# Kernel tuning notes

Hardware: AMD Instinct MI355X
Metric: run time of the kernel (lower is better)

Reference implementation:

```python
import jax, jax.numpy as jnp
import numpy as np

B, N, H = 32, 1024, 256
ALPHA = 0.2  # leaky relu slope
NEG_INF = -1e12


def setup_inputs() -> dict:
    key = jax.random.key(0)
    k1, k2, k3, k4, k5, k6 = jax.random.split(key, 6)
    inp = jax.random.normal(k1, (B, N, H), dtype=jnp.float32)
    A = (jax.random.uniform(k2, (B, N, N)) < 0.05).astype(jnp.float32)
    l = jnp.sort(jax.random.randint(k3, (B, 2), 0, N), axis=1)
    # xavier-uniform(gain=1.414) approximated; exact init values are irrelevant for correctness
    lim_w = 1.414 * np.sqrt(6.0 / (H + H))
    W_i = jax.random.uniform(k4, (H, H), minval=-lim_w, maxval=lim_w, dtype=jnp.float32)
    W_c = jax.random.uniform(k5, (H, H), minval=-lim_w, maxval=lim_w, dtype=jnp.float32)
    lim_a = 1.414 * np.sqrt(6.0 / (2 * H + 1))
    a = jax.random.uniform(k6, (2 * H, 1), minval=-lim_a, maxval=lim_a, dtype=jnp.float32)
    return {"inp": inp, "A": A, "l": l, "W_i": W_i, "W_c": W_c, "a": a}


def reference(inp, A, l, W_i, W_c, a):
    # eval mode: dropout is identity (training=False)
    n = inp.shape[1]
    h = inp.shape[2]
    Wh_i = jnp.einsum('bnh,he->bne', inp, W_i)
    Wh_c = jnp.einsum('bnh,he->bne', inp, W_c)
    # vectorized replacement of the per-batch Wh[index][i:j] = Wh_i[index][i:j] loop
    idx = jnp.arange(n)
    sel = (idx[None, :] >= l[:, 0:1]) & (idx[None, :] < l[:, 1:2])  # [B,N]
    Wh = jnp.where(sel[:, :, None], Wh_i, Wh_c)
    # additive attention scores
    Wh1 = Wh @ a[:h, :]  # [B,N,1]
    Wh2 = Wh @ a[h:, :]  # [B,N,1]
    A_ = A + jnp.eye(n, dtype=A.dtype)
    e = jax.nn.leaky_relu((Wh1 + jnp.swapaxes(Wh2, 1, 2)) * A_, ALPHA)
    att = jnp.where(A_ > 0, e, NEG_INF)
    att = jax.nn.softmax(att, axis=2)
    h_prime = jnp.einsum('bnm,bme->bne', att, Wh)
    return jax.nn.elu(h_prime)  # concat=True
```

## Files before the change

### kernel.cpp

```cpp
#include <hip/hip_runtime.h>
#include <hip/hip_bf16.h>
#include <stdint.h>

#define B_ 32
#define N_ 1024
#define H_ 256
#define PF_PITCH 520

typedef short bf16x8 __attribute__((ext_vector_type(8)));
typedef float floatx4 __attribute__((ext_vector_type(4)));

__device__ inline unsigned short f2bs(float x) {
    __hip_bfloat16 h = __float2bfloat16(x);
    return __builtin_bit_cast(unsigned short, h);
}

__global__ __launch_bounds__(256)
void k_pre(const float* __restrict__ Wi, const float* __restrict__ Wc,
           const float* __restrict__ a, float* __restrict__ U,
           unsigned short* __restrict__ WtFi, unsigned short* __restrict__ WtFc) {
    int bid = blockIdx.x;
    int t = threadIdx.x;
    if (bid < 32) {
        __shared__ float tile[64][65];
        int mat = bid >> 4;
        int tr = ((bid >> 2) & 3) * 64;
        int tc = (bid & 3) * 64;
        const float* W = mat ? Wc : Wi;
        unsigned short* WtF = mat ? WtFc : WtFi;
        int rr = t >> 2, c4 = (t & 3) * 16;
        const float* src = W + (size_t)(tr + rr) * H_ + tc + c4;
#pragma unroll
        for (int j = 0; j < 4; ++j) {
            float4 v = *reinterpret_cast<const float4*>(src + j * 4);
            tile[rr][c4 + 4 * j + 0] = v.x;
            tile[rr][c4 + 4 * j + 1] = v.y;
            tile[rr][c4 + 4 * j + 2] = v.z;
            tile[rr][c4 + 4 * j + 3] = v.w;
        }
        __syncthreads();
#pragma unroll
        for (int h = 0; h < 2; ++h) {
            int s = h * 256 + t;
            int ksl = s >> 8;
            int cl  = (s >> 6) & 3;
            int ll  = s & 63;
            int m16v = ll & 15, quadv = ll >> 4;
            int nloc = cl * 16 + m16v;
            int kb = ksl * 32 + quadv * 8;
            unsigned int pk[4];
#pragma unroll
            for (int jj = 0; jj < 4; ++jj) {
                unsigned short lo = f2bs(tile[kb + 2 * jj][nloc]);
                unsigned short hi = f2bs(tile[kb + 2 * jj + 1][nloc]);
                pk[jj] = (unsigned int)lo | ((unsigned int)hi << 16);
            }
            int ksg = (tr >> 5) + ksl;
            int cg  = (tc >> 4) + cl;
            *reinterpret_cast<uint4*>(WtF + ((size_t)(ksg * 16 + cg) * 64 + ll) * 8) =
                *reinterpret_cast<uint4*>(pk);
        }
    } else {
        int k = bid - 32;
        float wi = Wi[k * H_ + t];
        float wc = Wc[k * H_ + t];
        float a1 = a[t], a2 = a[H_ + t];
        float p0 = wi * a1, p1 = wc * a1, p2 = wi * a2, p3 = wc * a2;
        for (int off = 32; off; off >>= 1) {
            p0 += __shfl_xor(p0, off);
            p1 += __shfl_xor(p1, off);
            p2 += __shfl_xor(p2, off);
            p3 += __shfl_xor(p3, off);
        }
        __shared__ float red[4][4];
        int w = t >> 6;
        if ((t & 63) == 0) { red[w][0] = p0; red[w][1] = p1; red[w][2] = p2; red[w][3] = p3; }
        __syncthreads();
        if (t == 0) {
            U[0 * H_ + k] = red[0][0] + red[1][0] + red[2][0] + red[3][0];
            U[1 * H_ + k] = red[0][1] + red[1][1] + red[2][1] + red[3][1];
            U[2 * H_ + k] = red[0][2] + red[1][2] + red[2][2] + red[3][2];
            U[3 * H_ + k] = red[0][3] + red[1][3] + red[2][3] + red[3][3];
        }
    }
}

__global__ __launch_bounds__(256)
void k_abits(const float* __restrict__ A, unsigned int* __restrict__ M) {
    int t = threadIdx.x;
    size_t row = (size_t)blockIdx.x * 8 + (t >> 5);
    int cd = t & 31;
    const float* src = A + row * N_ + cd * 32;
    float4 v[8];
#pragma unroll
    for (int j = 0; j < 8; ++j)
        v[j] = *reinterpret_cast<const float4*>(src + j * 4);
    unsigned int bits = 0;
#pragma unroll
    for (int j = 0; j < 8; ++j) {
        bits |= (v[j].x > 0.f ? 1u : 0u) << (j * 4 + 0);
        bits |= (v[j].y > 0.f ? 1u : 0u) << (j * 4 + 1);
        bits |= (v[j].z > 0.f ? 1u : 0u) << (j * 4 + 2);
        bits |= (v[j].w > 0.f ? 1u : 0u) << (j * 4 + 3);
    }
    M[row * 32 + cd] = bits;
}

__global__ __launch_bounds__(256, 2)
void k_gemm(const float* __restrict__ inp, const int* __restrict__ l,
            const unsigned short* __restrict__ WtFi, const unsigned short* __restrict__ WtFc,
            unsigned short* __restrict__ WhF, const float* __restrict__ U,
            float* __restrict__ Wh1, float* __restrict__ Wh2) {
    __shared__ unsigned short bbuf[2][8192];
    int blk = blockIdx.x;
    int b  = blk >> 4;
    int r0 = (blk & 15) * 64;
    int t = threadIdx.x;
    int w = t >> 6;
    int lane = t & 63;
    int quad = lane >> 4, m16 = lane & 15;
    int rowb = r0 + w * 16;

    int l0 = l[2 * b], l1 = l[2 * b + 1];
    bool allI = (l0 <= r0) && (r0 + 64 <= l1);
    bool allC = (l1 <= r0) || (l0 >= r0 + 64);
    int npass = (allI || allC) ? 1 : 2;

    int row = rowb + m16;
    bool sel = (row >= l0) && (row < l1);
    const float* xrow = inp + ((size_t)(b * N_ + row)) * H_;
    const float* u1 = U + (sel ? 0 : H_);
    const float* u2 = U + 2 * H_ + (sel ? 0 : H_);

    float d1 = 0.f, d2 = 0.f;
#pragma unroll 2
    for (int ks = 0; ks < 8; ++ks) {
        const float4 xa = *reinterpret_cast<const float4*>(xrow + ks * 32 + quad * 8);
        const float4 xb = *reinterpret_cast<const float4*>(xrow + ks * 32 + quad * 8 + 4);
        const float4 ua = *reinterpret_cast<const float4*>(u1 + ks * 32 + quad * 8);
        const float4 ub = *reinterpret_cast<const float4*>(u1 + ks * 32 + quad * 8 + 4);
        const float4 va = *reinterpret_cast<const float4*>(u2 + ks * 32 + quad * 8);
        const float4 vb = *reinterpret_cast<const float4*>(u2 + ks * 32 + quad * 8 + 4);
        d1 += xa.x * ua.x + xa.y * ua.y + xa.z * ua.z + xa.w * ua.w
            + xb.x * ub.x + xb.y * ub.y + xb.z * ub.z + xb.w * ub.w;
        d2 += xa.x * va.x + xa.y * va.y + xa.z * va.z + xa.w * va.w
            + xb.x * vb.x + xb.y * vb.y + xb.z * vb.z + xb.w * vb.w;
    }
    d1 += __shfl_xor(d1, 16); d1 += __shfl_xor(d1, 32);
    d2 += __shfl_xor(d2, 16); d2 += __shfl_xor(d2, 32);
    if (quad == 0) {
        Wh1[b * N_ + rowb + m16] = d1;
        Wh2[b * N_ + rowb + m16] = d2;
    }

    unsigned short* fb = WhF + (size_t)b * (N_ * H_);
    int j0 = rowb + quad * 4;
    int ksO = j0 >> 5;
    int laneF = m16 + 16 * ((j0 & 31) >> 3);
    int jj0 = j0 & 7;

    for (int pass = 0; pass < npass; ++pass) {
        const unsigned short* gbase =
            (npass == 1) ? (allI ? WtFi : WtFc) : (pass == 0 ? WtFi : WtFc);

        floatx4 acc[16];
#pragma unroll
        for (int c = 0; c < 16; ++c) acc[c] = (floatx4){0.f, 0.f, 0.f, 0.f};

        {
#pragma unroll
            for (int j = 0; j < 4; ++j)
                *reinterpret_cast<uint4*>(&bbuf[0][j * 2048 + t * 8]) =
                    *reinterpret_cast<const uint4*>(gbase + j * 2048 + t * 8);
        }
        for (int ks = 0; ks < 8; ++ks) {
            __syncthreads();
            uint4 v[4];
            if (ks < 7) {
                const unsigned short* sn = gbase + (size_t)(ks + 1) * 8192;
#pragma unroll
                for (int j = 0; j < 4; ++j)
                    v[j] = *reinterpret_cast<const uint4*>(sn + j * 2048 + t * 8);
            }
            const float4 xa = *reinterpret_cast<const float4*>(xrow + ks * 32 + quad * 8);
            const float4 xb = *reinterpret_cast<const float4*>(xrow + ks * 32 + quad * 8 + 4);
            unsigned int pk0 = (unsigned int)f2bs(xa.x) | ((unsigned int)f2bs(xa.y) << 16);
            unsigned int pk1 = (unsigned int)f2bs(xa.z) | ((unsigned int)f2bs(xa.w) << 16);
            unsigned int pk2 = (unsigned int)f2bs(xb.x) | ((unsigned int)f2bs(xb.y) << 16);
            unsigned int pk3 = (unsigned int)f2bs(xb.z) | ((unsigned int)f2bs(xb.w) << 16);
            uint4 apk = {pk0, pk1, pk2, pk3};
            bf16x8 af = __builtin_bit_cast(bf16x8, apk);

            const unsigned short* bptr = &bbuf[ks & 1][lane * 8];
#pragma unroll
            for (int c = 0; c < 16; ++c) {
                bf16x8 bfr = *reinterpret_cast<const bf16x8*>(bptr + c * 512);
                acc[c] = __builtin_amdgcn_mfma_f32_16x16x32_bf16(af, bfr, acc[c], 0, 0, 0);
            }
            if (ks < 7) {
#pragma unroll
                for (int j = 0; j < 4; ++j)
                    *reinterpret_cast<uint4*>(&bbuf[(ks + 1) & 1][j * 2048 + t * 8]) = v[j];
            }
        }
        __syncthreads();

#pragma unroll
        for (int c = 0; c < 16; ++c) {
            size_t base = ((size_t)((ksO * 16 + c) * 64) + laneF) * 8 + jj0;
            if (npass == 1) {
                unsigned int lo = (unsigned int)f2bs(acc[c][0]) | ((unsigned int)f2bs(acc[c][1]) << 16);
                unsigned int hi = (unsigned int)f2bs(acc[c][2]) | ((unsigned int)f2bs(acc[c][3]) << 16);
                uint2 v2 = {lo, hi};
                *reinterpret_cast<uint2*>(fb + base) = v2;
            } else {
                bool want[4]; bool all = true, none = true;
#pragma unroll
                for (int r = 0; r < 4; ++r) {
                    int j = j0 + r;
                    bool s2 = (j >= l0) && (j < l1);
                    want[r] = (pass == 0) ? s2 : !s2;
                    all = all && want[r]; none = none && !want[r];
                }
                if (all) {
                    unsigned int lo = (unsigned int)f2bs(acc[c][0]) | ((unsigned int)f2bs(acc[c][1]) << 16);
                    unsigned int hi = (unsigned int)f2bs(acc[c][2]) | ((unsigned int)f2bs(acc[c][3]) << 16);
                    uint2 v2 = {lo, hi};
                    *reinterpret_cast<uint2*>(fb + base) = v2;
                } else if (!none) {
#pragma unroll
                    for (int r = 0; r < 4; ++r)
                        if (want[r]) fb[base + r] = f2bs(acc[c][r]);
                }
            }
        }
    }
}

__global__ __launch_bounds__(256)
void k_attn(const unsigned int* __restrict__ Mask, const float* __restrict__ Wh1,
            const float* __restrict__ Wh2, const unsigned short* __restrict__ WhF,
            float* __restrict__ out) {
    __shared__ unsigned short pfrag[2][32 * PF_PITCH];
    __shared__ float rsum[2][16];
    int t = threadIdx.x, w = t >> 6, lane = t & 63;
    int bi = blockIdx.x;
    int b = (bi & 7) * 4 + (bi >> 8);
    int tile = (bi >> 3) & 31;
    int rowbase = tile * 32;

    const float* Wh2b = Wh2 + b * N_;
    float4 w2v[4];
#pragma unroll
    for (int ch = 0; ch < 4; ++ch)
        w2v[ch] = *reinterpret_cast<const float4*>(Wh2b + ch * 256 + lane * 4);

    int ksl = lane >> 3;
    int q2 = (lane >> 1) & 3;
    int jj0 = (lane & 1) * 4;
    int mdw = lane >> 3;
    int msh = (lane & 7) * 4;

#pragma unroll
    for (int tt = 0; tt < 2; ++tt) {
#pragma unroll
        for (int q = 0; q < 4; ++q) {
            int m = w * 4 + q;
            int i = rowbase + tt * 16 + m;
            float wh1 = Wh1[b * N_ + i];
            const unsigned int* Mrow = Mask + ((size_t)(b * N_ + i)) * 32;
            unsigned int mr[4];
#pragma unroll
            for (int ch = 0; ch < 4; ++ch)
                mr[ch] = Mrow[ch * 8 + mdw];
            int s = m + 16 * q2;
            int sw = s ^ ((s >> 3) & 7);
            int sls = sw * 8 + jj0;
            float rp = 0.f;
#pragma unroll
            for (int ch = 0; ch < 4; ++ch) {
                float aa[4];
#pragma unroll
                for (int c = 0; c < 4; ++c)
                    aa[c] = (float)((mr[ch] >> (msh + c)) & 1u);
                if ((i >> 2) == (ch * 64 + lane)) aa[i & 3] += 1.0f;
                float ww[4] = {w2v[ch].x, w2v[ch].y, w2v[ch].z, w2v[ch].w};
                float p[4];
#pragma unroll
                for (int c = 0; c < 4; ++c) {
                    float e  = (wh1 + ww[c]) * aa[c];
                    float lv = fmaxf(e, 0.2f * e);
                    p[c] = aa[c] > 0.f ? __expf(lv) : 0.f;
                }
                rp += (p[0] + p[1]) + (p[2] + p[3]);
                unsigned int lo = (unsigned int)f2bs(p[0]) | ((unsigned int)f2bs(p[1]) << 16);
                unsigned int hi = (unsigned int)f2bs(p[2]) | ((unsigned int)f2bs(p[3]) << 16);
                uint2 v = {lo, hi};
                int ks = ch * 8 + ksl;
                *reinterpret_cast<uint2*>(pfrag[tt] + ks * PF_PITCH + sls) = v;
            }
            for (int off = 32; off; off >>= 1) rp += __shfl_xor(rp, off);
            if (lane == 0) rsum[tt][m] = rp;
        }
    }
    __syncthreads();

    const unsigned short* WB = WhF + (size_t)b * (N_ * H_);
    int rs = (lane ^ ((lane >> 3) & 7)) * 8;
    floatx4 acc0[4], acc1[4];
#pragma unroll
    for (int cc = 0; cc < 4; ++cc) {
        acc0[cc] = (floatx4){0.f, 0.f, 0.f, 0.f};
        acc1[cc] = (floatx4){0.f, 0.f, 0.f, 0.f};
    }
    bf16x8 af0 = *reinterpret_cast<const bf16x8*>(pfrag[0] + rs);
    bf16x8 af1 = *reinterpret_cast<const bf16x8*>(pfrag[1] + rs);
    bf16x8 bfv[4];
#pragma unroll
    for (int cc = 0; cc < 4; ++cc)
        bfv[cc] = *reinterpret_cast<const bf16x8*>(
            WB + ((size_t)((w * 4 + cc) * 64 + lane)) * 8);
    for (int ks = 0; ks < 32; ++ks) {
        bf16x8 naf0, naf1, nbf[4];
        if (ks < 31) {
            naf0 = *reinterpret_cast<const bf16x8*>(pfrag[0] + (ks + 1) * PF_PITCH + rs);
            naf1 = *reinterpret_cast<const bf16x8*>(pfrag[1] + (ks + 1) * PF_PITCH + rs);
#pragma unroll
            for (int cc = 0; cc < 4; ++cc)
                nbf[cc] = *reinterpret_cast<const bf16x8*>(
                    WB + ((size_t)(((ks + 1) * 16 + w * 4 + cc) * 64 + lane)) * 8);
        }
#pragma unroll
        for (int cc = 0; cc < 4; ++cc) {
            acc0[cc] = __builtin_amdgcn_mfma_f32_16x16x32_bf16(af0, bfv[cc], acc0[cc], 0, 0, 0);
            acc1[cc] = __builtin_amdgcn_mfma_f32_16x16x32_bf16(af1, bfv[cc], acc1[cc], 0, 0, 0);
        }
        if (ks < 31) {
            af0 = naf0; af1 = naf1;
#pragma unroll
            for (int cc = 0; cc < 4; ++cc) bfv[cc] = nbf[cc];
        }
    }

    int quad = lane >> 4, m16 = lane & 15;
    float inv0[4], inv1[4];
#pragma unroll
    for (int r = 0; r < 4; ++r) {
        inv0[r] = 1.0f / rsum[0][quad * 4 + r];
        inv1[r] = 1.0f / rsum[1][quad * 4 + r];
    }
#pragma unroll
    for (int cc = 0; cc < 4; ++cc) {
        int col = (w * 4 + cc) * 16 + m16;
#pragma unroll
        for (int r = 0; r < 4; ++r) {
            int m = quad * 4 + r;
            float v0 = acc0[cc][r] * inv0[r];
            v0 = v0 > 0.f ? v0 : __expf(v0) - 1.0f;
            out[((size_t)(b * N_ + rowbase + m)) * H_ + col] = v0;
            float v1 = acc1[cc][r] * inv1[r];
            v1 = v1 > 0.f ? v1 : __expf(v1) - 1.0f;
            out[((size_t)(b * N_ + rowbase + 16 + m)) * H_ + col] = v1;
        }
    }
}

extern "C" void kernel_launch(void* const* d_in, const int* in_sizes, int n_in,
                              void* d_out, int out_size, void* d_ws, size_t ws_size,
                              hipStream_t stream) {
    const float* inp = (const float*)d_in[0];
    const float* A   = (const float*)d_in[1];
    const int*   l   = (const int*)d_in[2];
    const float* Wi  = (const float*)d_in[3];
    const float* Wc  = (const float*)d_in[4];
    const float* a   = (const float*)d_in[5];
    float* out = (float*)d_out;

    char* ws = (char*)d_ws;
    size_t off = 0;
    unsigned short* WhF  = (unsigned short*)(ws + off); off += (size_t)B_ * N_ * H_ * 2;
    float* Wh1 = (float*)(ws + off); off += (size_t)B_ * N_ * 4;
    float* Wh2 = (float*)(ws + off); off += (size_t)B_ * N_ * 4;
    float* U   = (float*)(ws + off); off += 4 * H_ * 4;
    unsigned short* WtFi = (unsigned short*)(ws + off); off += (size_t)H_ * H_ * 2;
    unsigned short* WtFc = (unsigned short*)(ws + off); off += (size_t)H_ * H_ * 2;
    unsigned int* Mask = (unsigned int*)(ws + off); off += (size_t)B_ * N_ * 32 * 4;

    k_pre<<<32 + H_, 256, 0, stream>>>(Wi, Wc, a, U, WtFi, WtFc);
    k_abits<<<(B_ * N_) / 8, 256, 0, stream>>>(A, Mask);
    k_gemm<<<B_ * 16, 256, 0, stream>>>(inp, l, WtFi, WtFc, WhF, U, Wh1, Wh2);
    k_attn<<<B_ * (N_ / 32), 256, 0, stream>>>(Mask, Wh1, Wh2, WhF, out);
}
```

Before: 295.1 us.

## Split GEMM output columns across two blocks and fuse Wh1/Wh2 dot into k-loop

Each k_gemm block now computes 128 of the 256 output columns, doubling the grid to 1024 blocks with half the accumulators and half the shared-memory staging buffer. The Wh1/Wh2 projection dots are folded into the main k-loop and done only by the column-0 block, which removes a separate pass over the input row. This aims to raise occupancy and parallelism for a small GEMM stage. In exchange, the input row is read and converted to bf16 twice, once per column half, and the launch-bounds occupancy hint is dropped.

```diff
diff --git a/kernel.cpp b/kernel.cpp
--- a/kernel.cpp
+++ b/kernel.cpp
@@ -106,15 +106,16 @@
     M[row * 32 + cd] = bits;
 }
 
-__global__ __launch_bounds__(256, 2)
+__global__ __launch_bounds__(256)
 void k_gemm(const float* __restrict__ inp, const int* __restrict__ l,
             const unsigned short* __restrict__ WtFi, const unsigned short* __restrict__ WtFc,
             unsigned short* __restrict__ WhF, const float* __restrict__ U,
             float* __restrict__ Wh1, float* __restrict__ Wh2) {
-    __shared__ unsigned short bbuf[2][8192];
+    __shared__ unsigned short bbuf[2][4096];
     int blk = blockIdx.x;
-    int b  = blk >> 4;
-    int r0 = (blk & 15) * 64;
+    int b  = blk >> 5;
+    int r0 = ((blk >> 1) & 15) * 64;
+    int n0 = (blk & 1) * 128;
     int t = threadIdx.x;
     int w = t >> 6;
     int lane = t & 63;
@@ -131,59 +132,51 @@
     const float* xrow = inp + ((size_t)(b * N_ + row)) * H_;
     const float* u1 = U + (sel ? 0 : H_);
     const float* u2 = U + 2 * H_ + (sel ? 0 : H_);
-
+    bool doWh = (n0 == 0);
     float d1 = 0.f, d2 = 0.f;
-#pragma unroll 2
-    for (int ks = 0; ks < 8; ++ks) {
-        const float4 xa = *reinterpret_cast<const float4*>(xrow + ks * 32 + quad * 8);
-        const float4 xb = *reinterpret_cast<const float4*>(xrow + ks * 32 + quad * 8 + 4);
-        const float4 ua = *reinterpret_cast<const float4*>(u1 + ks * 32 + quad * 8);
-        const float4 ub = *reinterpret_cast<const float4*>(u1 + ks * 32 + quad * 8 + 4);
-        const float4 va = *reinterpret_cast<const float4*>(u2 + ks * 32 + quad * 8);
-        const float4 vb = *reinterpret_cast<const float4*>(u2 + ks * 32 + quad * 8 + 4);
-        d1 += xa.x * ua.x + xa.y * ua.y + xa.z * ua.z + xa.w * ua.w
-            + xb.x * ub.x + xb.y * ub.y + xb.z * ub.z + xb.w * ub.w;
-        d2 += xa.x * va.x + xa.y * va.y + xa.z * va.z + xa.w * va.w
-            + xb.x * vb.x + xb.y * vb.y + xb.z * vb.z + xb.w * vb.w;
-    }
-    d1 += __shfl_xor(d1, 16); d1 += __shfl_xor(d1, 32);
-    d2 += __shfl_xor(d2, 16); d2 += __shfl_xor(d2, 32);
-    if (quad == 0) {
-        Wh1[b * N_ + rowb + m16] = d1;
-        Wh2[b * N_ + rowb + m16] = d2;
-    }
 
     unsigned short* fb = WhF + (size_t)b * (N_ * H_);
+    int cb = n0 >> 4;
+
     int j0 = rowb + quad * 4;
     int ksO = j0 >> 5;
     int laneF = m16 + 16 * ((j0 & 31) >> 3);
     int jj0 = j0 & 7;
 
     for (int pass = 0; pass < npass; ++pass) {
-        const unsigned short* gbase =
+        const unsigned short* WtF =
             (npass == 1) ? (allI ? WtFi : WtFc) : (pass == 0 ? WtFi : WtFc);
-
-        floatx4 acc[16];
-#pragma unroll
-        for (int c = 0; c < 16; ++c) acc[c] = (floatx4){0.f, 0.f, 0.f, 0.f};
+        const unsigned short* gbase = WtF + cb * 512;
+
+        floatx4 acc[8];
+#pragma unroll
+        for (int c = 0; c < 8; ++c) acc[c] = (floatx4){0.f, 0.f, 0.f, 0.f};
 
         {
-#pragma unroll
-            for (int j = 0; j < 4; ++j)
-                *reinterpret_cast<uint4*>(&bbuf[0][j * 2048 + t * 8]) =
-                    *reinterpret_cast<const uint4*>(gbase + j * 2048 + t * 8);
+            uint4 v0 = *reinterpret_cast<const uint4*>(gbase + (size_t)t * 8);
+            uint4 v1 = *reinterpret_cast<const uint4*>(gbase + (size_t)(256 + t) * 8);
+            *reinterpret_cast<uint4*>(&bbuf[0][t * 8]) = v0;
+            *reinterpret_cast<uint4*>(&bbuf[0][(256 + t) * 8]) = v1;
         }
         for (int ks = 0; ks < 8; ++ks) {
             __syncthreads();
-            uint4 v[4];
+            uint4 v0, v1;
             if (ks < 7) {
-                const unsigned short* sn = gbase + (size_t)(ks + 1) * 8192;
-#pragma unroll
-                for (int j = 0; j < 4; ++j)
-                    v[j] = *reinterpret_cast<const uint4*>(sn + j * 2048 + t * 8);
+                v0 = *reinterpret_cast<const uint4*>(gbase + (size_t)(ks + 1) * 8192 + t * 8);
+                v1 = *reinterpret_cast<const uint4*>(gbase + (size_t)(ks + 1) * 8192 + (256 + t) * 8);
             }
             const float4 xa = *reinterpret_cast<const float4*>(xrow + ks * 32 + quad * 8);
             const float4 xb = *reinterpret_cast<const float4*>(xrow + ks * 32 + quad * 8 + 4);
+            if (pass == 0 && doWh) {
+                const float4 ua = *reinterpret_cast<const float4*>(u1 + ks * 32 + quad * 8);
+                const float4 ub = *reinterpret_cast<const float4*>(u1 + ks * 32 + quad * 8 + 4);
+                const float4 va = *reinterpret_cast<const float4*>(u2 + ks * 32 + quad * 8);
+                const float4 vb = *reinterpret_cast<const float4*>(u2 + ks * 32 + quad * 8 + 4);
+                d1 += xa.x * ua.x + xa.y * ua.y + xa.z * ua.z + xa.w * ua.w
+                    + xb.x * ub.x + xb.y * ub.y + xb.z * ub.z + xb.w * ub.w;
+                d2 += xa.x * va.x + xa.y * va.y + xa.z * va.z + xa.w * va.w
+                    + xb.x * vb.x + xb.y * vb.y + xb.z * vb.z + xb.w * vb.w;
+            }
             unsigned int pk0 = (unsigned int)f2bs(xa.x) | ((unsigned int)f2bs(xa.y) << 16);
             unsigned int pk1 = (unsigned int)f2bs(xa.z) | ((unsigned int)f2bs(xa.w) << 16);
             unsigned int pk2 = (unsigned int)f2bs(xb.x) | ((unsigned int)f2bs(xb.y) << 16);
@@ -193,26 +186,25 @@
 
             const unsigned short* bptr = &bbuf[ks & 1][lane * 8];
 #pragma unroll
-            for (int c = 0; c < 16; ++c) {
+            for (int c = 0; c < 8; ++c) {
                 bf16x8 bfr = *reinterpret_cast<const bf16x8*>(bptr + c * 512);
                 acc[c] = __builtin_amdgcn_mfma_f32_16x16x32_bf16(af, bfr, acc[c], 0, 0, 0);
             }
             if (ks < 7) {
-#pragma unroll
-                for (int j = 0; j < 4; ++j)
-                    *reinterpret_cast<uint4*>(&bbuf[(ks + 1) & 1][j * 2048 + t * 8]) = v[j];
+                *reinterpret_cast<uint4*>(&bbuf[(ks + 1) & 1][t * 8]) = v0;
+                *reinterpret_cast<uint4*>(&bbuf[(ks + 1) & 1][(256 + t) * 8]) = v1;
             }
         }
         __syncthreads();
 
 #pragma unroll
-        for (int c = 0; c < 16; ++c) {
-            size_t base = ((size_t)((ksO * 16 + c) * 64) + laneF) * 8 + jj0;
+        for (int c = 0; c < 8; ++c) {
+            size_t base = ((size_t)((ksO * 16 + cb + c) * 64) + laneF) * 8 + jj0;
             if (npass == 1) {
                 unsigned int lo = (unsigned int)f2bs(acc[c][0]) | ((unsigned int)f2bs(acc[c][1]) << 16);
                 unsigned int hi = (unsigned int)f2bs(acc[c][2]) | ((unsigned int)f2bs(acc[c][3]) << 16);
-                uint2 v2 = {lo, hi};
-                *reinterpret_cast<uint2*>(fb + base) = v2;
+                uint2 v = {lo, hi};
+                *reinterpret_cast<uint2*>(fb + base) = v;
             } else {
                 bool want[4]; bool all = true, none = true;
 #pragma unroll
@@ -225,14 +217,23 @@
                 if (all) {
                     unsigned int lo = (unsigned int)f2bs(acc[c][0]) | ((unsigned int)f2bs(acc[c][1]) << 16);
                     unsigned int hi = (unsigned int)f2bs(acc[c][2]) | ((unsigned int)f2bs(acc[c][3]) << 16);
-                    uint2 v2 = {lo, hi};
-                    *reinterpret_cast<uint2*>(fb + base) = v2;
+                    uint2 v = {lo, hi};
+                    *reinterpret_cast<uint2*>(fb + base) = v;
                 } else if (!none) {
 #pragma unroll
                     for (int r = 0; r < 4; ++r)
                         if (want[r]) fb[base + r] = f2bs(acc[c][r]);
                 }
             }
+        }
+    }
+
+    if (doWh) {
+        d1 += __shfl_xor(d1, 16); d1 += __shfl_xor(d1, 32);
+        d2 += __shfl_xor(d2, 16); d2 += __shfl_xor(d2, 32);
+        if (quad == 0) {
+            Wh1[b * N_ + rowb + m16] = d1;
+            Wh2[b * N_ + rowb + m16] = d2;
         }
     }
 }
@@ -388,6 +389,6 @@
 
     k_pre<<<32 + H_, 256, 0, stream>>>(Wi, Wc, a, U, WtFi, WtFc);
     k_abits<<<(B_ * N_) / 8, 256, 0, stream>>>(A, Mask);
-    k_gemm<<<B_ * 16, 256, 0, stream>>>(inp, l, WtFi, WtFc, WhF, U, Wh1, Wh2);
+    k_gemm<<<B_ * 16 * 2, 256, 0, stream>>>(inp, l, WtFi, WtFc, WhF, U, Wh1, Wh2);
     k_attn<<<B_ * (N_ / 32), 256, 0, stream>>>(Mask, Wh1, Wh2, WhF, out);
 }
```

Measured after the change: 289.8 us. Within noise of the previous version (-1.8%).
